# Performance work log

Hardware: AMD Instinct MI355X
Metric: run time of the kernel (lower is better)

The kernel has to match this reference:

```python
import jax, jax.numpy as jnp
import numpy as np

N_NODES = 100000
N_EDGES = 1600000
IN_CH = 128
HID_CH = 128   # 2 * out_channels
OUT_CH = 64


def gcn_conv(x, edge_index, W, b):
    """PyG GCNConv: x @ W, add self-loops, symmetric deg^-1/2 norm, scatter-sum, + bias."""
    n = x.shape[0]
    xw = x @ W                                   # [N, F_out]
    loop = jnp.arange(n, dtype=edge_index.dtype)
    row = jnp.concatenate([edge_index[0], loop])  # source nodes
    col = jnp.concatenate([edge_index[1], loop])  # target nodes (aggregation)
    deg = jax.ops.segment_sum(jnp.ones_like(col, dtype=xw.dtype), col, num_segments=n)
    dinv = jnp.where(deg > 0, jax.lax.rsqrt(deg), 0.0)
    norm = dinv[row] * dinv[col]                 # [E+N]
    msg = xw[row] * norm[:, None]                # gather + scale
    out = jax.ops.segment_sum(msg, col, num_segments=n)
    return out + b


def setup_inputs() -> dict:
    key = jax.random.key(0)
    k1, k2, k3, k4, k5 = jax.random.split(key, 5)
    x = jax.random.normal(k1, (N_NODES, IN_CH), dtype=jnp.float32)
    edge_index = jax.random.randint(k2, (2, N_EDGES), 0, N_NODES, dtype=jnp.int32)
    # Glorot-style init for GCN weights
    W1 = jax.random.normal(k3, (IN_CH, HID_CH), dtype=jnp.float32) * (1.0 / np.sqrt(IN_CH))
    b1 = jnp.zeros((HID_CH,), dtype=jnp.float32)
    W2 = jax.random.normal(k4, (HID_CH, OUT_CH), dtype=jnp.float32) * (1.0 / np.sqrt(HID_CH))
    b2 = jnp.zeros((OUT_CH,), dtype=jnp.float32)
    return {"x": x, "edge_index": edge_index, "W1": W1, "b1": b1, "W2": W2, "b2": b2}


def reference(x, edge_index, W1, b1, W2, b2):
    h = jax.nn.relu(gcn_conv(x, edge_index, W1, b1))
    return gcn_conv(h, edge_index, W2, b2)
```

## Files before the change

kernel.cpp:

```cpp
#include <hip/hip_runtime.h>


typedef unsigned int uint;

#define BKT_SH 7
#define BKT    (1 << BKT_SH)
#define NBUCK_MAX 1024
#define CHUNK 16384

__device__ __forceinline__ float bf_lo(uint v) { return __uint_as_float(v << 16); }
__device__ __forceinline__ float bf_hi(uint v) { return __uint_as_float(v & 0xffff0000u); }
__device__ __forceinline__ uint pack_bf16(float x, float y) {
    uint bx = __float_as_uint(x), by = __float_as_uint(y);
    bx += 0x7fffu + ((bx >> 16) & 1u);
    by += 0x7fffu + ((by >> 16) & 1u);
    return (bx >> 16) | (by & 0xffff0000u);
}


__global__ __launch_bounds__(1024) void scan_a(const int* __restrict__ in,
                                               int* __restrict__ outp,
                                               int* __restrict__ bsums, int n) {
    __shared__ int s[2][1024];
    int t = threadIdx.x;
    int i = blockIdx.x * 1024 + t;
    int v = (i < n) ? in[i] : 0;
    s[0][t] = v;
    __syncthreads();
    int p = 0;
    for (int d = 1; d < 1024; d <<= 1) {
        int val = s[p][t] + ((t >= d) ? s[p][t - d] : 0);
        s[p ^ 1][t] = val;
        p ^= 1;
        __syncthreads();
    }
    if (i < n) outp[i] = s[p][t] - v;
    if (t == 1023) bsums[blockIdx.x] = s[p][t];
}

__global__ __launch_bounds__(256) void scan_b(int* __restrict__ bsums, int nb) {
    __shared__ int s[2][256];
    int t = threadIdx.x;
    int v = (t < nb) ? bsums[t] : 0;
    s[0][t] = v;
    __syncthreads();
    int p = 0;
    for (int d = 1; d < 256; d <<= 1) {
        int val = s[p][t] + ((t >= d) ? s[p][t - d] : 0);
        s[p ^ 1][t] = val;
        p ^= 1;
        __syncthreads();
    }
    if (t < nb) bsums[t] = s[p][t] - v;
}

__global__ __launch_bounds__(256) void scan_c(int* __restrict__ outp,
                                              const int* __restrict__ bsums, int n, int total) {
    int i = blockIdx.x * 256 + threadIdx.x;
    if (i < n)       outp[i] += bsums[i >> 10];
    else if (i == n) outp[n] = total;
}


__global__ __launch_bounds__(256) void bucket_hist(const int* __restrict__ col,
                                                   int* __restrict__ lhist,
                                                   int E, int nbuck, int nblk) {
    __shared__ int sh[NBUCK_MAX];
    int t = threadIdx.x;
    for (int b = t; b < nbuck; b += 256) sh[b] = 0;
    __syncthreads();
    const int4* c4 = (const int4*)col;
    int i4base = blockIdx.x * (CHUNK / 4);
    int E4 = E >> 2;
#pragma unroll
    for (int it = 0; it < CHUNK / 4 / 256; ++it) {
        int i4 = i4base + it * 256 + t;
        if (i4 < E4) {
            int4 c = c4[i4];
            atomicAdd(&sh[c.x >> BKT_SH], 1);
            atomicAdd(&sh[c.y >> BKT_SH], 1);
            atomicAdd(&sh[c.z >> BKT_SH], 1);
            atomicAdd(&sh[c.w >> BKT_SH], 1);
        }
    }
    if (blockIdx.x == 0 && t < (E & 3)) atomicAdd(&sh[col[(E & ~3) + t] >> BKT_SH], 1);
    __syncthreads();
    for (int b = t; b < nbuck; b += 256) lhist[b * nblk + blockIdx.x] = sh[b];
}


__global__ __launch_bounds__(256) void partition_kernel(const int* __restrict__ row,
                                                        const int* __restrict__ col,
                                                        const int* __restrict__ loff,
                                                        uint2* __restrict__ part,
                                                        int E, int nbuck, int nblk) {
    __shared__ int cur[NBUCK_MAX];
    int t = threadIdx.x;
    for (int b = t; b < nbuck; b += 256) cur[b] = loff[b * nblk + blockIdx.x];
    __syncthreads();
    const int4* c4 = (const int4*)col;
    const int4* r4 = (const int4*)row;
    int i4base = blockIdx.x * (CHUNK / 4);
    int E4 = E >> 2;
#pragma unroll
    for (int it = 0; it < CHUNK / 4 / 256; ++it) {
        int i4 = i4base + it * 256 + t;
        if (i4 < E4) {
            int4 c = c4[i4];
            int4 r = r4[i4];
            int p0 = atomicAdd(&cur[c.x >> BKT_SH], 1); part[p0] = make_uint2((uint)c.x, (uint)r.x);
            int p1 = atomicAdd(&cur[c.y >> BKT_SH], 1); part[p1] = make_uint2((uint)c.y, (uint)r.y);
            int p2 = atomicAdd(&cur[c.z >> BKT_SH], 1); part[p2] = make_uint2((uint)c.z, (uint)r.z);
            int p3 = atomicAdd(&cur[c.w >> BKT_SH], 1); part[p3] = make_uint2((uint)c.w, (uint)r.w);
        }
    }
    if (blockIdx.x == 0 && t < (E & 3)) {
        int e = (E & ~3) + t;
        int c = col[e];
        int p = atomicAdd(&cur[c >> BKT_SH], 1);
        part[p] = make_uint2((uint)c, (uint)row[e]);
    }
}


__global__ __launch_bounds__(256) void fill2(const uint2* __restrict__ part,
                                             const int* __restrict__ loff,
                                             int* __restrict__ rp,
                                             float* __restrict__ dinv,
                                             int* __restrict__ csr,
                                             int E, int nbuck, int nblk, int N) {
    __shared__ int lcnt[BKT];
    __shared__ int sc[2][BKT];
    __shared__ int lbase[BKT];
    __shared__ int lcur[BKT];
    int b = blockIdx.x;
    int t = threadIdx.x;
    if (t < BKT) lcnt[t] = 0;
    __syncthreads();

    int beg = b * nblk < nbuck * nblk ? loff[b * nblk] : E;
    int end = (b + 1 < nbuck) ? loff[(b + 1) * nblk] : E;

    for (int e = beg + t; e < end; e += 256) {
        uint2 pr = part[e];
        atomicAdd(&lcnt[(int)pr.x & (BKT - 1)], 1);
    }
    __syncthreads();

    int myv = (t < BKT) ? lcnt[t] : 0;
    if (t < BKT) sc[0][t] = myv;
    __syncthreads();
    int p = 0;
    for (int d = 1; d < BKT; d <<= 1) {
        if (t < BKT) {
            int val = sc[p][t] + ((t >= d) ? sc[p][t - d] : 0);
            sc[p ^ 1][t] = val;
        }
        p ^= 1;
        __syncthreads();
    }
    if (t < BKT) {
        int base = beg + sc[p][t] - myv;
        lbase[t] = base;
        lcur[t]  = 0;
        int c = (b << BKT_SH) + t;
        if (c <= N)  rp[c] = base;
        if (c < N)   dinv[c] = rsqrtf((float)(myv + 1));
    }
    __syncthreads();

    for (int e = beg + t; e < end; e += 256) {
        uint2 pr = part[e];
        int cl = (int)pr.x & (BKT - 1);
        int slot = atomicAdd(&lcur[cl], 1);
        csr[lbase[cl] + slot] = (int)pr.y;
    }
}


template <int NC, bool BF16_IN>
__global__ __launch_bounds__(256) void gemm_scale(const void* __restrict__ Xv,
                                                  const float* __restrict__ W,
                                                  const float* __restrict__ dinv,
                                                  uint* __restrict__ out, int M) {
    constexpr int K = 128, BM = 64, PAD = 132, CPT = NC / 16;
    __shared__ float xs[BM * PAD];
    __shared__ float ws[32 * NC];

    int tid = threadIdx.x;
    int block_row = blockIdx.x * BM;

    if (BF16_IN) {
        const uint* X = (const uint*)Xv;
        int r = tid >> 5, c = tid & 31;
#pragma unroll
        for (int p = 0; p < 8; ++p) {
            int rr = r + p * 8;
            int gr = block_row + rr;
            if (gr > M - 1) gr = M - 1;
            uint2 v = *(const uint2*)(X + (size_t)gr * 64 + c * 2);
            float* d = xs + rr * PAD + c * 4;
            d[0] = bf_lo(v.x); d[1] = bf_hi(v.x);
            d[2] = bf_lo(v.y); d[3] = bf_hi(v.y);
        }
    } else {
        const float* X = (const float*)Xv;
        int r = tid >> 5, k4 = tid & 31;
#pragma unroll
        for (int p = 0; p < 8; ++p) {
            int rr = r + p * 8;
            int gr = block_row + rr;
            if (gr > M - 1) gr = M - 1;
            float4 v = *(const float4*)(X + (size_t)gr * K + k4 * 4);
            *(float4*)(xs + rr * PAD + k4 * 4) = v;
        }
    }

    int tc = tid & 15;
    int tr = tid >> 4;

    float acc[4][CPT];
#pragma unroll
    for (int i = 0; i < 4; ++i)
#pragma unroll
        for (int j = 0; j < CPT; ++j) acc[i][j] = 0.0f;

    for (int kc = 0; kc < K / 32; ++kc) {
        {
            const float4* src = (const float4*)(W + (size_t)kc * 32 * NC);
            float4* dst = (float4*)ws;
#pragma unroll
            for (int i = 0; i < NC / 32; ++i) dst[tid + i * 256] = src[tid + i * 256];
        }
        __syncthreads();

#pragma unroll 2
        for (int k4 = 0; k4 < 8; ++k4) {
            float4 xa[4];
#pragma unroll
            for (int i = 0; i < 4; ++i)
                xa[i] = *(const float4*)(xs + (tr * 4 + i) * PAD + kc * 32 + k4 * 4);
#pragma unroll
            for (int kk = 0; kk < 4; ++kk) {
                float wv[CPT];
#pragma unroll
                for (int m = 0; m < CPT / 4; ++m) {
                    float4 w4 = *(const float4*)(ws + (k4 * 4 + kk) * NC + tc * CPT + m * 4);
                    wv[m * 4 + 0] = w4.x; wv[m * 4 + 1] = w4.y;
                    wv[m * 4 + 2] = w4.z; wv[m * 4 + 3] = w4.w;
                }
#pragma unroll
                for (int i = 0; i < 4; ++i) {
                    float xv = (&xa[i].x)[kk];
#pragma unroll
                    for (int j = 0; j < CPT; ++j) acc[i][j] = fmaf(xv, wv[j], acc[i][j]);
                }
            }
        }
        __syncthreads();
    }

#pragma unroll
    for (int i = 0; i < 4; ++i) {
        int r = block_row + tr * 4 + i;
        if (r < M) {
            float di = dinv[r];
            if (CPT == 8) {
                uint4 o;
                o.x = pack_bf16(acc[i][0] * di, acc[i][1] * di);
                o.y = pack_bf16(acc[i][2] * di, acc[i][3] * di);
                o.z = pack_bf16(acc[i][4] * di, acc[i][5] * di);
                o.w = pack_bf16(acc[i][6] * di, acc[i][7] * di);
                *(uint4*)(out + (size_t)r * 64 + tc * 4) = o;
            } else {
                uint2 o;
                o.x = pack_bf16(acc[i][0] * di, acc[i][1] * di);
                o.y = pack_bf16(acc[i][2] * di, acc[i][3] * di);
                *(uint2*)(out + (size_t)r * 32 + tc * 2) = o;
            }
        }
    }
}


__global__ __launch_bounds__(256) void agg128(const uint* __restrict__ xws,
                                              const int* __restrict__ rp,
                                              const int* __restrict__ csr,
                                              const float* __restrict__ dinv,
                                              const float* __restrict__ bias,
                                              uint* __restrict__ h, int n) {
    int gid  = blockIdx.x * 256 + threadIdx.x;
    int node = gid >> 6;
    int lane = gid & 63;
    if (node >= n) return;

    uint self = xws[(size_t)node * 64 + lane];
    float ax = bf_lo(self), ay = bf_hi(self);

    int beg = rp[node], end = rp[node + 1];
    int e = beg;
    for (; e + 8 <= end; e += 8) {
        int s0 = csr[e],     s1 = csr[e + 1], s2 = csr[e + 2], s3 = csr[e + 3];
        int s4 = csr[e + 4], s5 = csr[e + 5], s6 = csr[e + 6], s7 = csr[e + 7];
        uint v0 = xws[(size_t)s0 * 64 + lane];
        uint v1 = xws[(size_t)s1 * 64 + lane];
        uint v2 = xws[(size_t)s2 * 64 + lane];
        uint v3 = xws[(size_t)s3 * 64 + lane];
        uint v4 = xws[(size_t)s4 * 64 + lane];
        uint v5 = xws[(size_t)s5 * 64 + lane];
        uint v6 = xws[(size_t)s6 * 64 + lane];
        uint v7 = xws[(size_t)s7 * 64 + lane];
        ax += bf_lo(v0) + bf_lo(v1) + bf_lo(v2) + bf_lo(v3)
            + bf_lo(v4) + bf_lo(v5) + bf_lo(v6) + bf_lo(v7);
        ay += bf_hi(v0) + bf_hi(v1) + bf_hi(v2) + bf_hi(v3)
            + bf_hi(v4) + bf_hi(v5) + bf_hi(v6) + bf_hi(v7);
    }
    if (e + 4 <= end) {
        int s0 = csr[e], s1 = csr[e + 1], s2 = csr[e + 2], s3 = csr[e + 3];
        uint v0 = xws[(size_t)s0 * 64 + lane];
        uint v1 = xws[(size_t)s1 * 64 + lane];
        uint v2 = xws[(size_t)s2 * 64 + lane];
        uint v3 = xws[(size_t)s3 * 64 + lane];
        ax += bf_lo(v0) + bf_lo(v1) + bf_lo(v2) + bf_lo(v3);
        ay += bf_hi(v0) + bf_hi(v1) + bf_hi(v2) + bf_hi(v3);
        e += 4;
    }
    for (; e < end; ++e) {
        uint v = xws[(size_t)csr[e] * 64 + lane];
        ax += bf_lo(v);
        ay += bf_hi(v);
    }

    float  di = dinv[node];
    float2 b  = ((const float2*)bias)[lane];
    float ox = fmaxf(fmaf(di, ax, b.x), 0.0f);
    float oy = fmaxf(fmaf(di, ay, b.y), 0.0f);
    h[(size_t)node * 64 + lane] = pack_bf16(ox, oy);
}

__global__ __launch_bounds__(256) void agg64(const uint* __restrict__ xws,
                                             const int* __restrict__ rp,
                                             const int* __restrict__ csr,
                                             const float* __restrict__ dinv,
                                             const float* __restrict__ bias,
                                             float* __restrict__ out, int n) {
    int gid  = blockIdx.x * 256 + threadIdx.x;
    int node = gid >> 5;
    int l    = gid & 31;
    if (node >= n) return;

    uint self = xws[(size_t)node * 32 + l];
    float ax = bf_lo(self), ay = bf_hi(self);

    int beg = rp[node], end = rp[node + 1];
    int e = beg;
    for (; e + 8 <= end; e += 8) {
        int s0 = csr[e],     s1 = csr[e + 1], s2 = csr[e + 2], s3 = csr[e + 3];
        int s4 = csr[e + 4], s5 = csr[e + 5], s6 = csr[e + 6], s7 = csr[e + 7];
        uint v0 = xws[(size_t)s0 * 32 + l];
        uint v1 = xws[(size_t)s1 * 32 + l];
        uint v2 = xws[(size_t)s2 * 32 + l];
        uint v3 = xws[(size_t)s3 * 32 + l];
        uint v4 = xws[(size_t)s4 * 32 + l];
        uint v5 = xws[(size_t)s5 * 32 + l];
        uint v6 = xws[(size_t)s6 * 32 + l];
        uint v7 = xws[(size_t)s7 * 32 + l];
        ax += bf_lo(v0) + bf_lo(v1) + bf_lo(v2) + bf_lo(v3)
            + bf_lo(v4) + bf_lo(v5) + bf_lo(v6) + bf_lo(v7);
        ay += bf_hi(v0) + bf_hi(v1) + bf_hi(v2) + bf_hi(v3)
            + bf_hi(v4) + bf_hi(v5) + bf_hi(v6) + bf_hi(v7);
    }
    if (e + 4 <= end) {
        int s0 = csr[e], s1 = csr[e + 1], s2 = csr[e + 2], s3 = csr[e + 3];
        uint v0 = xws[(size_t)s0 * 32 + l];
        uint v1 = xws[(size_t)s1 * 32 + l];
        uint v2 = xws[(size_t)s2 * 32 + l];
        uint v3 = xws[(size_t)s3 * 32 + l];
        ax += bf_lo(v0) + bf_lo(v1) + bf_lo(v2) + bf_lo(v3);
        ay += bf_hi(v0) + bf_hi(v1) + bf_hi(v2) + bf_hi(v3);
        e += 4;
    }
    for (; e < end; ++e) {
        uint v = xws[(size_t)csr[e] * 32 + l];
        ax += bf_lo(v);
        ay += bf_hi(v);
    }

    float  di = dinv[node];
    float2 b  = ((const float2*)bias)[l];
    float2 o;
    o.x = fmaf(di, ax, b.x);
    o.y = fmaf(di, ay, b.y);
    ((float2*)out)[(size_t)node * 32 + l] = o;
}


static inline size_t align512(size_t x) { return (x + 511) & ~(size_t)511; }

extern "C" void kernel_launch(void* const* d_in, const int* in_sizes, int n_in,
                              void* d_out, int out_size, void* d_ws, size_t ws_size,
                              hipStream_t stream) {
    const float* x   = (const float*)d_in[0];
    const int*   ei  = (const int*)d_in[1];
    const float* W1  = (const float*)d_in[2];
    const float* b1  = (const float*)d_in[3];
    const float* W2  = (const float*)d_in[4];
    const float* b2  = (const float*)d_in[5];
    float*       out = (float*)d_out;

    const int N = in_sizes[0] / 128;
    const int E = in_sizes[1] / 2;
    const int* row = ei;
    const int* col = ei + E;

    const int nbuck = (N + BKT - 1) >> BKT_SH;
    const int nblk  = (E + CHUNK - 1) / CHUNK;
    const int L     = nbuck * nblk;

    char* w = (char*)d_ws;
    size_t off = 0;
    auto take = [&](size_t bytes) { void* p = w + off; off = align512(off + bytes); return p; };
    int*   rp     = (int*)  take((size_t)(N + 1) * 4);
    int*   bsums  = (int*)  take(4096);
    float* dinv   = (float*)take((size_t)N * 4);
    int*   csr    = (int*)  take((size_t)E * 4);
    uint*  xws    = (uint*) take((size_t)N * 64 * 4);
    uint*  h      = (uint*) take((size_t)N * 64 * 4);
    (void)ws_size;
    int*   lhist = (int*)xws;
    int*   loff  = (int*)xws + L + 128;
    uint2* part  = (uint2*)h;

    bucket_hist<<<nblk, 256, 0, stream>>>(col, lhist, E, nbuck, nblk);
    int nb2 = (L + 1023) / 1024;
    scan_a<<<nb2, 1024, 0, stream>>>(lhist, loff, bsums, L);
    scan_b<<<1, 256, 0, stream>>>(bsums, nb2);
    scan_c<<<(L + 256) / 256, 256, 0, stream>>>(loff, bsums, L, E);
    partition_kernel<<<nblk, 256, 0, stream>>>(row, col, loff, part, E, nbuck, nblk);
    fill2<<<nbuck, 256, 0, stream>>>(part, loff, rp, dinv, csr, E, nbuck, nblk, N);

    gemm_scale<128, false><<<(N + 63) / 64, 256, 0, stream>>>(x, W1, dinv, xws, N);
    agg128<<<(N + 3) / 4, 256, 0, stream>>>(xws, rp, csr, dinv, b1, h, N);

    gemm_scale<64, true><<<(N + 63) / 64, 256, 0, stream>>>(h, W2, dinv, xws, N);
    agg64<<<(N + 7) / 8, 256, 0, stream>>>(xws, rp, csr, dinv, b2, out, N);
}
```

Before: 332.3 us.

## Fold scan fixup into consumers, halve partition chunk, widen gather unroll, restripe GEMM columns

The scan_c launch is removed: partition and fill2 now add the block-sum offsets themselves when they read the scanned local offsets. CHUNK is halved, so bucket_hist and partition launch twice as many blocks. The GEMM now gives each thread interleaved column groups (tc + m*16) so shared-memory reads and bf16 stores are strided rather than contiguous per thread. agg128 unrolls its gather to 16 edges at a time, and agg64 moves to array-based 8-wide loops. The goal is less launch overhead, more parallelism in partitioning and more memory-level parallelism in the gathers, at the cost of larger histogram and offset arrays and more register pressure.

```diff
diff --git a/kernel.cpp b/kernel.cpp
--- a/kernel.cpp
+++ b/kernel.cpp
@@ -6,7 +6,7 @@
 #define BKT_SH 7
 #define BKT    (1 << BKT_SH)
 #define NBUCK_MAX 1024
-#define CHUNK 16384
+#define CHUNK 8192
 
 __device__ __forceinline__ float bf_lo(uint v) { return __uint_as_float(v << 16); }
 __device__ __forceinline__ float bf_hi(uint v) { return __uint_as_float(v & 0xffff0000u); }
@@ -54,13 +54,6 @@
     if (t < nb) bsums[t] = s[p][t] - v;
 }
 
-__global__ __launch_bounds__(256) void scan_c(int* __restrict__ outp,
-                                              const int* __restrict__ bsums, int n, int total) {
-    int i = blockIdx.x * 256 + threadIdx.x;
-    if (i < n)       outp[i] += bsums[i >> 10];
-    else if (i == n) outp[n] = total;
-}
-
 
 __global__ __launch_bounds__(256) void bucket_hist(const int* __restrict__ col,
                                                    int* __restrict__ lhist,
@@ -88,15 +81,18 @@
     for (int b = t; b < nbuck; b += 256) lhist[b * nblk + blockIdx.x] = sh[b];
 }
 
-
 __global__ __launch_bounds__(256) void partition_kernel(const int* __restrict__ row,
                                                         const int* __restrict__ col,
                                                         const int* __restrict__ loff,
+                                                        const int* __restrict__ bsums,
                                                         uint2* __restrict__ part,
                                                         int E, int nbuck, int nblk) {
     __shared__ int cur[NBUCK_MAX];
     int t = threadIdx.x;
-    for (int b = t; b < nbuck; b += 256) cur[b] = loff[b * nblk + blockIdx.x];
+    for (int b = t; b < nbuck; b += 256) {
+        int idx = b * nblk + blockIdx.x;
+        cur[b] = loff[idx] + bsums[idx >> 10];
+    }
     __syncthreads();
     const int4* c4 = (const int4*)col;
     const int4* r4 = (const int4*)row;
@@ -125,6 +121,7 @@
 
 __global__ __launch_bounds__(256) void fill2(const uint2* __restrict__ part,
                                              const int* __restrict__ loff,
+                                             const int* __restrict__ bsums,
                                              int* __restrict__ rp,
                                              float* __restrict__ dinv,
                                              int* __restrict__ csr,
@@ -138,8 +135,13 @@
     if (t < BKT) lcnt[t] = 0;
     __syncthreads();
 
-    int beg = b * nblk < nbuck * nblk ? loff[b * nblk] : E;
-    int end = (b + 1 < nbuck) ? loff[(b + 1) * nblk] : E;
+    int i0  = b * nblk;
+    int beg = loff[i0] + bsums[i0 >> 10];
+    int end = E;
+    if (b + 1 < nbuck) {
+        int i1 = (b + 1) * nblk;
+        end = loff[i1] + bsums[i1 >> 10];
+    }
 
     for (int e = beg + t; e < end; e += 256) {
         uint2 pr = part[e];
@@ -245,7 +247,7 @@
                 float wv[CPT];
 #pragma unroll
                 for (int m = 0; m < CPT / 4; ++m) {
-                    float4 w4 = *(const float4*)(ws + (k4 * 4 + kk) * NC + tc * CPT + m * 4);
+                    float4 w4 = *(const float4*)(ws + (k4 * 4 + kk) * NC + (tc + m * 16) * 4);
                     wv[m * 4 + 0] = w4.x; wv[m * 4 + 1] = w4.y;
                     wv[m * 4 + 2] = w4.z; wv[m * 4 + 3] = w4.w;
                 }
@@ -265,18 +267,12 @@
         int r = block_row + tr * 4 + i;
         if (r < M) {
             float di = dinv[r];
-            if (CPT == 8) {
-                uint4 o;
-                o.x = pack_bf16(acc[i][0] * di, acc[i][1] * di);
-                o.y = pack_bf16(acc[i][2] * di, acc[i][3] * di);
-                o.z = pack_bf16(acc[i][4] * di, acc[i][5] * di);
-                o.w = pack_bf16(acc[i][6] * di, acc[i][7] * di);
-                *(uint4*)(out + (size_t)r * 64 + tc * 4) = o;
-            } else {
+#pragma unroll
+            for (int m = 0; m < CPT / 4; ++m) {
                 uint2 o;
-                o.x = pack_bf16(acc[i][0] * di, acc[i][1] * di);
-                o.y = pack_bf16(acc[i][2] * di, acc[i][3] * di);
-                *(uint2*)(out + (size_t)r * 32 + tc * 2) = o;
+                o.x = pack_bf16(acc[i][m * 4 + 0] * di, acc[i][m * 4 + 1] * di);
+                o.y = pack_bf16(acc[i][m * 4 + 2] * di, acc[i][m * 4 + 3] * di);
+                *(uint2*)(out + (size_t)r * (NC / 2) + (tc + m * 16) * 2) = o;
             }
         }
     }
@@ -299,21 +295,26 @@
 
     int beg = rp[node], end = rp[node + 1];
     int e = beg;
-    for (; e + 8 <= end; e += 8) {
-        int s0 = csr[e],     s1 = csr[e + 1], s2 = csr[e + 2], s3 = csr[e + 3];
-        int s4 = csr[e + 4], s5 = csr[e + 5], s6 = csr[e + 6], s7 = csr[e + 7];
-        uint v0 = xws[(size_t)s0 * 64 + lane];
-        uint v1 = xws[(size_t)s1 * 64 + lane];
-        uint v2 = xws[(size_t)s2 * 64 + lane];
-        uint v3 = xws[(size_t)s3 * 64 + lane];
-        uint v4 = xws[(size_t)s4 * 64 + lane];
-        uint v5 = xws[(size_t)s5 * 64 + lane];
-        uint v6 = xws[(size_t)s6 * 64 + lane];
-        uint v7 = xws[(size_t)s7 * 64 + lane];
-        ax += bf_lo(v0) + bf_lo(v1) + bf_lo(v2) + bf_lo(v3)
-            + bf_lo(v4) + bf_lo(v5) + bf_lo(v6) + bf_lo(v7);
-        ay += bf_hi(v0) + bf_hi(v1) + bf_hi(v2) + bf_hi(v3)
-            + bf_hi(v4) + bf_hi(v5) + bf_hi(v6) + bf_hi(v7);
+    for (; e + 16 <= end; e += 16) {
+        int s[16];
+#pragma unroll
+        for (int q = 0; q < 16; ++q) s[q] = csr[e + q];
+        uint v[16];
+#pragma unroll
+        for (int q = 0; q < 16; ++q) v[q] = xws[(size_t)s[q] * 64 + lane];
+#pragma unroll
+        for (int q = 0; q < 16; ++q) { ax += bf_lo(v[q]); ay += bf_hi(v[q]); }
+    }
+    if (e + 8 <= end) {
+        int s[8];
+#pragma unroll
+        for (int q = 0; q < 8; ++q) s[q] = csr[e + q];
+        uint v[8];
+#pragma unroll
+        for (int q = 0; q < 8; ++q) v[q] = xws[(size_t)s[q] * 64 + lane];
+#pragma unroll
+        for (int q = 0; q < 8; ++q) { ax += bf_lo(v[q]); ay += bf_hi(v[q]); }
+        e += 8;
     }
     if (e + 4 <= end) {
         int s0 = csr[e], s1 = csr[e + 1], s2 = csr[e + 2], s3 = csr[e + 3];
@@ -355,20 +356,14 @@
     int beg = rp[node], end = rp[node + 1];
     int e = beg;
     for (; e + 8 <= end; e += 8) {
-        int s0 = csr[e],     s1 = csr[e + 1], s2 = csr[e + 2], s3 = csr[e + 3];
-        int s4 = csr[e + 4], s5 = csr[e + 5], s6 = csr[e + 6], s7 = csr[e + 7];
-        uint v0 = xws[(size_t)s0 * 32 + l];
-        uint v1 = xws[(size_t)s1 * 32 + l];
-        uint v2 = xws[(size_t)s2 * 32 + l];
-        uint v3 = xws[(size_t)s3 * 32 + l];
-        uint v4 = xws[(size_t)s4 * 32 + l];
-        uint v5 = xws[(size_t)s5 * 32 + l];
-        uint v6 = xws[(size_t)s6 * 32 + l];
-        uint v7 = xws[(size_t)s7 * 32 + l];
-        ax += bf_lo(v0) + bf_lo(v1) + bf_lo(v2) + bf_lo(v3)
-            + bf_lo(v4) + bf_lo(v5) + bf_lo(v6) + bf_lo(v7);
-        ay += bf_hi(v0) + bf_hi(v1) + bf_hi(v2) + bf_hi(v3)
-            + bf_hi(v4) + bf_hi(v5) + bf_hi(v6) + bf_hi(v7);
+        int s[8];
+#pragma unroll
+        for (int q = 0; q < 8; ++q) s[q] = csr[e + q];
+        uint v[8];
+#pragma unroll
+        for (int q = 0; q < 8; ++q) v[q] = xws[(size_t)s[q] * 32 + l];
+#pragma unroll
+        for (int q = 0; q < 8; ++q) { ax += bf_lo(v[q]); ay += bf_hi(v[q]); }
     }
     if (e + 4 <= end) {
         int s0 = csr[e], s1 = csr[e + 1], s2 = csr[e + 2], s3 = csr[e + 3];
@@ -435,9 +430,8 @@
     int nb2 = (L + 1023) / 1024;
     scan_a<<<nb2, 1024, 0, stream>>>(lhist, loff, bsums, L);
     scan_b<<<1, 256, 0, stream>>>(bsums, nb2);
-    scan_c<<<(L + 256) / 256, 256, 0, stream>>>(loff, bsums, L, E);
-    partition_kernel<<<nblk, 256, 0, stream>>>(row, col, loff, part, E, nbuck, nblk);
-    fill2<<<nbuck, 256, 0, stream>>>(part, loff, rp, dinv, csr, E, nbuck, nblk, N);
+    partition_kernel<<<nblk, 256, 0, stream>>>(row, col, loff, bsums, part, E, nbuck, nblk);
+    fill2<<<nbuck, 256, 0, stream>>>(part, loff, bsums, rp, dinv, csr, E, nbuck, nblk, N);
 
     gemm_scale<128, false><<<(N + 63) / 64, 256, 0, stream>>>(x, W1, dinv, xws, N);
     agg128<<<(N + 3) / 4, 256, 0, stream>>>(xws, rp, csr, dinv, b1, h, N);
```

Measured after the change: 324.1 us. -2.5%, faster.
